# Kernel optimization log

Measured on AMD Instinct MI355X. Metric: run time of the kernel, lower is better.

## Reference

```python
import jax, jax.numpy as jnp
import numpy as np

N = 100000      # nodes
E = 2500000     # edges
DIN, H, DOUT = 3, 32, 4
EPS = 1e-5

def _lin(k, i, o):
    kw, kb = jax.random.split(k)
    lim = 1.0 / np.sqrt(i)
    W = jax.random.uniform(kw, (i, o), jnp.float32, -lim, lim)
    b = jax.random.uniform(kb, (o,), jnp.float32, -lim, lim)
    return W, b

def setup_inputs():
    key = jax.random.key(0)
    ks = jax.random.split(key, 12)
    x = jax.random.normal(ks[0], (N, DIN), jnp.float32)
    edge_index = jax.random.randint(ks[1], (2, E), 0, N, dtype=jnp.int32)
    w_in1, b_in1 = _lin(ks[2], DIN, H)
    w_in2, b_in2 = _lin(ks[3], H, H)
    gamma = jnp.ones((H,), jnp.float32)
    beta = jnp.zeros((H,), jnp.float32)
    wg1, bg1 = _lin(ks[4], H, H)
    wg2, bg2 = _lin(ks[5], H, H)
    wg3, bg3 = _lin(ks[6], H, H)
    wo1, bo1 = _lin(ks[7], H, H)
    wo2, bo2 = _lin(ks[8], H, H)
    wo3, bo3 = _lin(ks[9], H, DOUT)
    return dict(x=x, w_in1=w_in1, b_in1=b_in1, w_in2=w_in2, b_in2=b_in2,
                gamma=gamma, beta=beta,
                wg1=wg1, bg1=bg1, wg2=wg2, bg2=bg2, wg3=wg3, bg3=bg3,
                wo1=wo1, bo1=bo1, wo2=wo2, bo2=bo2, wo3=wo3, bo3=bo3,
                edge_index=edge_index)

def _gcn(h, W, b, src, dst, norm):
    # PyG GCNConv: x' = scatter_add(norm * (xW)[src] -> dst) + bias
    hw = h @ W                                   # [N, H]
    msg = hw[src] * norm[:, None]                # [E+N, H] gather + scale
    out = jax.ops.segment_sum(msg, dst, num_segments=N)
    return out + b

def reference(x, w_in1, b_in1, w_in2, b_in2, gamma, beta,
              wg1, bg1, wg2, bg2, wg3, bg3,
              wo1, bo1, wo2, bo2, wo3, bo3, edge_index):
    leaky = lambda v: jax.nn.leaky_relu(v, 0.01)
    # input MLP
    h = leaky(x @ w_in1 + b_in1)
    h = leaky(h @ w_in2 + b_in2)
    # BatchNorm1d (training-mode batch statistics, biased variance)
    mu = jnp.mean(h, axis=0)
    var = jnp.mean((h - mu) ** 2, axis=0)
    h = (h - mu) * jax.lax.rsqrt(var + EPS) * gamma + beta
    # gcn_norm with self-loops: deg over target index, sym normalization
    loop = jnp.arange(N, dtype=edge_index.dtype)
    src = jnp.concatenate([edge_index[0], loop])
    dst = jnp.concatenate([edge_index[1], loop])
    deg = jax.ops.segment_sum(jnp.ones_like(src, jnp.float32), dst, num_segments=N)
    dis = jax.lax.rsqrt(deg)                     # deg >= 1 due to self-loops
    norm = dis[src] * dis[dst]                   # [E+N]
    h = jax.nn.elu(_gcn(h, wg1, bg1, src, dst, norm))
    h = jax.nn.elu(_gcn(h, wg2, bg2, src, dst, norm))
    h = jax.nn.elu(_gcn(h, wg3, bg3, src, dst, norm))
    # output MLP
    r = leaky(h @ wo1 + bo1)
    r = leaky(r @ wo2 + bo2)
    r = r @ wo3 + bo3                            # [N, 4]
    r = r.at[:, 0].set(jax.nn.sigmoid(r[:, 0]))
    return r
```

## Files before the change

kernel.cpp:

```cpp
#include <hip/hip_runtime.h>
#include <hip/hip_fp16.h>

#define HF 32
#define EPS 1e-5f
#define BSH 8
#define BSZ 256
#define CH  4096
#define SUBCAP 1024
#define CAP (8*SUBCAP)

__device__ __forceinline__ float leaky(float v){ return fmaxf(v, 0.01f*v); }
__device__ __forceinline__ float elu1(float v){ return v > 0.f ? v : (expf(v)-1.f); }
__device__ __forceinline__ float sigmoidf(float v){ return 1.f/(1.f+expf(-v)); }

__device__ __forceinline__ void addrow8(float* a, float4 v){
    const __half2* p = (const __half2*)&v;
#pragma unroll
    for (int k = 0; k < 4; k++){
        float2 f = __half22float2(p[k]);
        a[2*k] += f.x; a[2*k+1] += f.y;
    }
}
__device__ __forceinline__ float4 h2add4f(float4 a, float4 b){
    __half2* pa = (__half2*)&a; __half2* pb = (__half2*)&b;
    float4 r; __half2* pr = (__half2*)&r;
#pragma unroll
    for (int k = 0; k < 4; k++) pr[k] = __hadd2(pa[k], pb[k]);
    return r;
}

__global__ __launch_bounds__(256)
void k_mlp(const float* __restrict__ x,
           const float* __restrict__ w1, const float* __restrict__ b1,
           const float* __restrict__ w2, const float* __restrict__ b2,
           __half* __restrict__ h, float* __restrict__ stats, int N){
    __shared__ float sW1[3*HF], sB1[HF], sW2[HF*HF], sB2[HF];
    __shared__ float sh[256][33];
    int t = threadIdx.x;
    for (int i = t; i < 3*HF; i += 256) sW1[i] = w1[i];
    if (t < HF){ sB1[t] = b1[t]; sB2[t] = b2[t]; }
    for (int i = t; i < HF*HF; i += 256) sW2[i] = w2[i];
    __syncthreads();
    int n = blockIdx.x*256 + t;
    float h2[HF];
    if (n < N){
        float x0 = x[(size_t)n*3], x1 = x[(size_t)n*3+1], x2 = x[(size_t)n*3+2];
        float h1[HF];
#pragma unroll
        for (int j = 0; j < HF; j++){
            float v = fmaf(x0, sW1[j], fmaf(x1, sW1[HF+j], fmaf(x2, sW1[2*HF+j], sB1[j])));
            h1[j] = leaky(v);
        }
#pragma unroll
        for (int j = 0; j < HF; j++){
            float v = sB2[j];
#pragma unroll
            for (int i = 0; i < HF; i++) v = fmaf(h1[i], sW2[i*HF+j], v);
            h2[j] = leaky(v);
        }
        float4* hv = (float4*)(h + (size_t)n*HF);
#pragma unroll
        for (int jb = 0; jb < 4; jb++){
            __half2 hh[4];
#pragma unroll
            for (int k = 0; k < 4; k++)
                hh[k] = __float22half2_rn(make_float2(h2[jb*8+2*k], h2[jb*8+2*k+1]));
            hv[jb] = *(float4*)hh;
        }
    } else {
#pragma unroll
        for (int j = 0; j < HF; j++) h2[j] = 0.f;
    }
#pragma unroll
    for (int j = 0; j < HF; j++) sh[t][j] = h2[j];
    __syncthreads();
    int f = t & 31, g = t >> 5;
    float s = 0.f, ss = 0.f;
    for (int i = 0; i < 32; i++){
        float v = sh[g*32 + i][f];
        s += v; ss += v*v;
    }
    __syncthreads();
    sh[g][f] = s; sh[8+g][f] = ss;
    __syncthreads();
    if (t < HF){
        float a = 0.f, b = 0.f;
#pragma unroll
        for (int g2 = 0; g2 < 8; g2++){ a += sh[g2][t]; b += sh[8+g2][t]; }
        atomicAdd(&stats[t], a);
        atomicAdd(&stats[HF+t], b);
    }
}

__global__ __launch_bounds__(256)
void k_bin(const int* __restrict__ src, const int* __restrict__ dst,
           int* __restrict__ gfill, int* __restrict__ ep, int E, int B){
    __shared__ int lcnt[512], lbase[512], lpos[512];
    int t = threadIdx.x;
    for (int i = t; i < B; i += 256){ lcnt[i] = 0; lpos[i] = 0; }
    __syncthreads();
    int base = blockIdx.x * CH;
    int xcd = blockIdx.x & 7;
#pragma unroll
    for (int i = 0; i < CH/1024; i++){
        int e = base + t + i*1024;
        int d0 = (e       < E) ? dst[e]       : -1;
        int d1 = (e+256   < E) ? dst[e+256]   : -1;
        int d2 = (e+512   < E) ? dst[e+512]   : -1;
        int d3 = (e+768   < E) ? dst[e+768]   : -1;
        if (d0 >= 0) atomicAdd(&lcnt[d0 >> BSH], 1);
        if (d1 >= 0) atomicAdd(&lcnt[d1 >> BSH], 1);
        if (d2 >= 0) atomicAdd(&lcnt[d2 >> BSH], 1);
        if (d3 >= 0) atomicAdd(&lcnt[d3 >> BSH], 1);
    }
    __syncthreads();
    for (int i = t; i < B; i += 256){
        int c = lcnt[i];
        lbase[i] = c ? (i*CAP + xcd*SUBCAP + atomicAdd(&gfill[i*8 + xcd], c)) : 0;
    }
    __syncthreads();
#pragma unroll
    for (int i = 0; i < CH/1024; i++){
        int e = base + t + i*1024;
#pragma unroll
        for (int k = 0; k < 4; k++){
            int ee = e + k*256;
            if (ee < E){
                int d = dst[ee], s = src[ee];
                int b = d >> BSH;
                int p = lbase[b] + atomicAdd(&lpos[b], 1);
                ep[p] = (s << BSH) | (d & (BSZ-1));
            }
        }
    }
}

__global__ __launch_bounds__(256)
void k_bucketD(int* __restrict__ ep, const int* __restrict__ gfill,
               int2* __restrict__ rowp2, float* __restrict__ dis, int N, int B){
    __shared__ int sep[CAP];
    __shared__ int lcnt[256], lpre[256], lfill[256], sc[256];
    int b = blockIdx.x, t = threadIdx.x;
    int cx[8], coff[8], cnt = 0;
#pragma unroll
    for (int x = 0; x < 8; x++){ cx[x] = gfill[b*8 + x]; coff[x] = cnt; cnt += cx[x]; }
    lcnt[t] = 0; lfill[t] = 0;
    __syncthreads();
    int base = b*CAP;
#pragma unroll
    for (int x = 0; x < 8; x++)
        for (int j = t; j < cx[x]; j += 256) sep[coff[x] + j] = ep[base + x*SUBCAP + j];
    __syncthreads();
    for (int e = t; e < cnt; e += 256) atomicAdd(&lcnt[sep[e] & (BSZ-1)], 1);
    __syncthreads();
    int v = lcnt[t];
    sc[t] = v; __syncthreads();
    for (int off = 1; off < 256; off <<= 1){
        int u = (t >= off) ? sc[t - off] : 0;
        __syncthreads();
        sc[t] += u;
        __syncthreads();
    }
    int pre = sc[t] - v;
    lpre[t] = pre;
    int n = b*BSZ + t;
    if (n < N){
        rowp2[n] = make_int2(base + pre, base + pre + v);
        dis[n]   = rsqrtf((float)(v + 1));
    }
    __syncthreads();
    for (int e = t; e < cnt; e += 256){
        int val = sep[e];
        int d = val & (BSZ-1);
        int p = lpre[d] + atomicAdd(&lfill[d], 1);
        ep[base + p] = val >> BSH;
    }
}

__global__ __launch_bounds__(256)
void k_bn_t1(const __half* __restrict__ h, const float* __restrict__ stats,
             const float* __restrict__ gamma, const float* __restrict__ beta,
             const float* __restrict__ W, const float* __restrict__ dis,
             __half* __restrict__ tout, int N){
    __shared__ float sW[HF*HF];
    __shared__ float sh[64][33];
    int tid = threadIdx.x;
    for (int i = tid; i < HF*HF; i += 256) sW[i] = W[i];
    int nib = tid >> 2, l = tid & 3;
    int n = blockIdx.x*64 + nib;
    float hv[8];
    float d = 0.f;
    if (n < N){
        float4 raw = ((const float4*)h)[(size_t)n*4 + l];
        const __half2* p = (const __half2*)&raw;
        float tmp[8];
#pragma unroll
        for (int k = 0; k < 4; k++){
            float2 f2 = __half22float2(p[k]);
            tmp[2*k] = f2.x; tmp[2*k+1] = f2.y;
        }
        d = dis[n];
        float inv = 1.0f / (float)N;
#pragma unroll
        for (int c = 0; c < 8; c++){
            int f = 8*l + c;
            float mu  = stats[f]    * inv;
            float var = stats[HF+f] * inv - mu*mu;
            float rs  = rsqrtf(var + EPS);
            hv[c] = (tmp[c] - mu) * rs * gamma[f] + beta[f];
        }
    } else {
#pragma unroll
        for (int c = 0; c < 8; c++) hv[c] = 0.f;
    }
    __syncthreads();
#pragma unroll
    for (int c = 0; c < 8; c++) sh[nib][8*l + c] = hv[c];
    __syncthreads();
    float o[8] = {0.f,0.f,0.f,0.f,0.f,0.f,0.f,0.f};
#pragma unroll
    for (int i = 0; i < HF; i++){
        float hvv = sh[nib][i];
        float4 w0 = *(const float4*)&sW[i*HF + 8*l];
        float4 w1 = *(const float4*)&sW[i*HF + 8*l + 4];
        o[0] = fmaf(hvv, w0.x, o[0]); o[1] = fmaf(hvv, w0.y, o[1]);
        o[2] = fmaf(hvv, w0.z, o[2]); o[3] = fmaf(hvv, w0.w, o[3]);
        o[4] = fmaf(hvv, w1.x, o[4]); o[5] = fmaf(hvv, w1.y, o[5]);
        o[6] = fmaf(hvv, w1.z, o[6]); o[7] = fmaf(hvv, w1.w, o[7]);
    }
    if (n < N){
        __half2 hh[4];
#pragma unroll
        for (int k = 0; k < 4; k++)
            hh[k] = __float22half2_rn(make_float2(o[2*k]*d, o[2*k+1]*d));
        ((float4*)tout)[(size_t)n*4 + l] = *(float4*)hh;
    }
}

__global__ __launch_bounds__(256)
void k_gather_t(const __half* __restrict__ tin, const int* __restrict__ esrc,
                const int2* __restrict__ rowp2, const float* __restrict__ dis,
                const float* __restrict__ bias, const float* __restrict__ W,
                __half* __restrict__ tout, int N){
    __shared__ float sW[HF*HF];
    __shared__ float sh[64][33];
    int tid = threadIdx.x;
    for (int i = tid; i < HF*HF; i += 256) sW[i] = W[i];
    int nib = tid >> 2, l = tid & 3;
    int n = blockIdx.x*64 + nib;
    float acc[8] = {0.f,0.f,0.f,0.f,0.f,0.f,0.f,0.f};
    float d = 0.f;
    const float4* tv = (const float4*)tin;
    if (n < N){
        addrow8(acc, tv[(size_t)n*4 + l]);
        int2 r = rowp2[n];
        int e = r.x, e1 = r.y;
        while (e < e1 && (e & 3)){ addrow8(acc, tv[(size_t)esrc[e]*4 + l]); e++; }
        for (; e + 3 < e1; e += 4){
            int4 s4 = *(const int4*)&esrc[e];
            float4 v0 = tv[(size_t)s4.x*4 + l];
            float4 v1 = tv[(size_t)s4.y*4 + l];
            float4 v2 = tv[(size_t)s4.z*4 + l];
            float4 v3 = tv[(size_t)s4.w*4 + l];
            addrow8(acc, h2add4f(h2add4f(v0, v1), h2add4f(v2, v3)));
        }
        for (; e < e1; e++) addrow8(acc, tv[(size_t)esrc[e]*4 + l]);
        d = dis[n];
#pragma unroll
        for (int c = 0; c < 8; c++)
            acc[c] = elu1(fmaf(d, acc[c], bias[8*l + c]));
    }
    __syncthreads();
#pragma unroll
    for (int c = 0; c < 8; c++) sh[nib][8*l + c] = acc[c];
    __syncthreads();
    float o[8] = {0.f,0.f,0.f,0.f,0.f,0.f,0.f,0.f};
#pragma unroll
    for (int i = 0; i < HF; i++){
        float hvv = sh[nib][i];
        float4 w0 = *(const float4*)&sW[i*HF + 8*l];
        float4 w1 = *(const float4*)&sW[i*HF + 8*l + 4];
        o[0] = fmaf(hvv, w0.x, o[0]); o[1] = fmaf(hvv, w0.y, o[1]);
        o[2] = fmaf(hvv, w0.z, o[2]); o[3] = fmaf(hvv, w0.w, o[3]);
        o[4] = fmaf(hvv, w1.x, o[4]); o[5] = fmaf(hvv, w1.y, o[5]);
        o[6] = fmaf(hvv, w1.z, o[6]); o[7] = fmaf(hvv, w1.w, o[7]);
    }
    if (n < N){
        __half2 hh[4];
#pragma unroll
        for (int k = 0; k < 4; k++)
            hh[k] = __float22half2_rn(make_float2(o[2*k]*d, o[2*k+1]*d));
        ((float4*)tout)[(size_t)n*4 + l] = *(float4*)hh;
    }
}

__global__ __launch_bounds__(256)
void k_gather_out(const __half* __restrict__ tin, const int* __restrict__ esrc,
                  const int2* __restrict__ rowp2, const float* __restrict__ dis,
                  const float* __restrict__ bg3,
                  const float* __restrict__ wo1, const float* __restrict__ bo1,
                  const float* __restrict__ wo2, const float* __restrict__ bo2,
                  const float* __restrict__ wo3, const float* __restrict__ bo3,
                  float* __restrict__ out, int N){
    __shared__ float sW1[HF*HF], sW2[HF*HF], sW3[HF*4];
    __shared__ float sh[64][33], sh2[64][33];
    int tid = threadIdx.x;
    for (int i = tid; i < HF*HF; i += 256){ sW1[i] = wo1[i]; sW2[i] = wo2[i]; }
    if (tid < HF*4) sW3[tid] = wo3[tid];
    int nib = tid >> 2, l = tid & 3;
    int n = blockIdx.x*64 + nib;
    float acc[8] = {0.f,0.f,0.f,0.f,0.f,0.f,0.f,0.f};
    const float4* tv = (const float4*)tin;
    if (n < N){
        addrow8(acc, tv[(size_t)n*4 + l]);
        int2 r = rowp2[n];
        int e = r.x, e1 = r.y;
        while (e < e1 && (e & 3)){ addrow8(acc, tv[(size_t)esrc[e]*4 + l]); e++; }
        for (; e + 3 < e1; e += 4){
            int4 s4 = *(const int4*)&esrc[e];
            float4 v0 = tv[(size_t)s4.x*4 + l];
            float4 v1 = tv[(size_t)s4.y*4 + l];
            float4 v2 = tv[(size_t)s4.z*4 + l];
            float4 v3 = tv[(size_t)s4.w*4 + l];
            addrow8(acc, h2add4f(h2add4f(v0, v1), h2add4f(v2, v3)));
        }
        for (; e < e1; e++) addrow8(acc, tv[(size_t)esrc[e]*4 + l]);
        float d = dis[n];
#pragma unroll
        for (int c = 0; c < 8; c++)
            acc[c] = elu1(fmaf(d, acc[c], bg3[8*l + c]));
    }
    __syncthreads();
#pragma unroll
    for (int c = 0; c < 8; c++) sh[nib][8*l + c] = acc[c];
    __syncthreads();
    float o1[8];
#pragma unroll
    for (int c = 0; c < 8; c++) o1[c] = bo1[8*l + c];
#pragma unroll
    for (int i = 0; i < HF; i++){
        float hvv = sh[nib][i];
        float4 w0 = *(const float4*)&sW1[i*HF + 8*l];
        float4 w1 = *(const float4*)&sW1[i*HF + 8*l + 4];
        o1[0] = fmaf(hvv, w0.x, o1[0]); o1[1] = fmaf(hvv, w0.y, o1[1]);
        o1[2] = fmaf(hvv, w0.z, o1[2]); o1[3] = fmaf(hvv, w0.w, o1[3]);
        o1[4] = fmaf(hvv, w1.x, o1[4]); o1[5] = fmaf(hvv, w1.y, o1[5]);
        o1[6] = fmaf(hvv, w1.z, o1[6]); o1[7] = fmaf(hvv, w1.w, o1[7]);
    }
#pragma unroll
    for (int c = 0; c < 8; c++) sh2[nib][8*l + c] = leaky(o1[c]);
    __syncthreads();
    float o2[8];
#pragma unroll
    for (int c = 0; c < 8; c++) o2[c] = bo2[8*l + c];
#pragma unroll
    for (int i = 0; i < HF; i++){
        float hvv = sh2[nib][i];
        float4 w0 = *(const float4*)&sW2[i*HF + 8*l];
        float4 w1 = *(const float4*)&sW2[i*HF + 8*l + 4];
        o2[0] = fmaf(hvv, w0.x, o2[0]); o2[1] = fmaf(hvv, w0.y, o2[1]);
        o2[2] = fmaf(hvv, w0.z, o2[2]); o2[3] = fmaf(hvv, w0.w, o2[3]);
        o2[4] = fmaf(hvv, w1.x, o2[4]); o2[5] = fmaf(hvv, w1.y, o2[5]);
        o2[6] = fmaf(hvv, w1.z, o2[6]); o2[7] = fmaf(hvv, w1.w, o2[7]);
    }
#pragma unroll
    for (int c = 0; c < 8; c++) sh[nib][8*l + c] = leaky(o2[c]);
    __syncthreads();
    if (n < N){
        float v = bo3[l];
#pragma unroll
        for (int i = 0; i < HF; i++) v = fmaf(sh[nib][i], sW3[i*4 + l], v);
        if (l == 0) v = sigmoidf(v);
        out[(size_t)n*4 + l] = v;
    }
}

extern "C" void kernel_launch(void* const* d_in, const int* in_sizes, int n_in,
                              void* d_out, int out_size, void* d_ws, size_t ws_size,
                              hipStream_t stream) {
    const float* x     = (const float*)d_in[0];
    const float* w_in1 = (const float*)d_in[1];
    const float* b_in1 = (const float*)d_in[2];
    const float* w_in2 = (const float*)d_in[3];
    const float* b_in2 = (const float*)d_in[4];
    const float* gamma = (const float*)d_in[5];
    const float* beta  = (const float*)d_in[6];
    const float* wg1   = (const float*)d_in[7];
    const float* bg1   = (const float*)d_in[8];
    const float* wg2   = (const float*)d_in[9];
    const float* bg2   = (const float*)d_in[10];
    const float* wg3   = (const float*)d_in[11];
    const float* bg3   = (const float*)d_in[12];
    const float* wo1   = (const float*)d_in[13];
    const float* bo1   = (const float*)d_in[14];
    const float* wo2   = (const float*)d_in[15];
    const float* bo2   = (const float*)d_in[16];
    const float* wo3   = (const float*)d_in[17];
    const float* bo3   = (const float*)d_in[18];
    const int*   ei    = (const int*)d_in[19];

    int N = in_sizes[0] / 3;
    int E = in_sizes[19] / 2;
    int B = (N + BSZ - 1) >> BSH;

    char* w = (char*)d_ws;
    size_t o = 0;
    auto alloc = [&](size_t bytes){ size_t r = o; o = (o + bytes + 255) & ~(size_t)255; return r; };
    float* stats = (float*)(w + alloc(2*HF*sizeof(float)));
    int*   gfill = (int*)  (w + alloc((size_t)B*8*4));
    size_t zero_bytes = o;
    int2*  rowp2 = (int2*) (w + alloc((size_t)N*8));
    float* dis   = (float*)(w + alloc((size_t)N*4));
    int*   ep    = (int*)  (w + alloc((size_t)B*CAP*4));
    __half* bufH = (__half*)(w + alloc((size_t)N*HF*2));
    __half* tA   = (__half*)(w + alloc((size_t)N*HF*2));
    __half* tB   = (__half*)(w + alloc((size_t)N*HF*2));

    hipMemsetAsync(d_ws, 0, zero_bytes, stream);

    const int* src = ei;
    const int* dst = ei + E;
    int NB1 = (N + 255) / 256;
    int NC  = (E + CH - 1) / CH;
    int GB  = (N + 63) / 64;

    k_mlp    <<<NB1, 256, 0, stream>>>(x, w_in1, b_in1, w_in2, b_in2, bufH, stats, N);
    k_bin    <<<NC,  256, 0, stream>>>(src, dst, gfill, ep, E, B);
    k_bucketD<<<B,   256, 0, stream>>>(ep, gfill, rowp2, dis, N, B);

    k_bn_t1   <<<GB, 256, 0, stream>>>(bufH, stats, gamma, beta, wg1, dis, tA, N);
    k_gather_t<<<GB, 256, 0, stream>>>(tA, ep, rowp2, dis, bg1, wg2, tB, N);
    k_gather_t<<<GB, 256, 0, stream>>>(tB, ep, rowp2, dis, bg2, wg3, tA, N);
    k_gather_out<<<GB, 256, 0, stream>>>(tA, ep, rowp2, dis, bg3,
                                         wo1, bo1, wo2, bo2, wo3, bo3, (float*)d_out, N);
}
```

Before: 314.6 us.

## Split feature columns into two half-planes for gather and separate dense transforms

Feature tensors are stored as two 16-column planes, and the gather kernel is split so each block aggregates one plane. Block indices are interleaved so a plane's gather traffic stays within a smaller working set that fits cache better. The 32x32 transforms and output MLP become separate kernels, which adds launches and extra round trips through memory. The binning kernel also preloads src/dst into registers once instead of reading dst twice.

```diff
diff --git a/kernel.cpp b/kernel.cpp
--- a/kernel.cpp
+++ b/kernel.cpp
@@ -101,18 +101,16 @@
     __syncthreads();
     int base = blockIdx.x * CH;
     int xcd = blockIdx.x & 7;
-#pragma unroll
-    for (int i = 0; i < CH/1024; i++){
-        int e = base + t + i*1024;
-        int d0 = (e       < E) ? dst[e]       : -1;
-        int d1 = (e+256   < E) ? dst[e+256]   : -1;
-        int d2 = (e+512   < E) ? dst[e+512]   : -1;
-        int d3 = (e+768   < E) ? dst[e+768]   : -1;
-        if (d0 >= 0) atomicAdd(&lcnt[d0 >> BSH], 1);
-        if (d1 >= 0) atomicAdd(&lcnt[d1 >> BSH], 1);
-        if (d2 >= 0) atomicAdd(&lcnt[d2 >> BSH], 1);
-        if (d3 >= 0) atomicAdd(&lcnt[d3 >> BSH], 1);
-    }
+    int dv[16], sv[16];
+#pragma unroll
+    for (int i = 0; i < 16; i++){
+        int e = base + t + i*256;
+        dv[i] = (e < E) ? dst[e] : -1;
+        sv[i] = (e < E) ? src[e] : 0;
+    }
+#pragma unroll
+    for (int i = 0; i < 16; i++)
+        if (dv[i] >= 0) atomicAdd(&lcnt[dv[i] >> BSH], 1);
     __syncthreads();
     for (int i = t; i < B; i += 256){
         int c = lcnt[i];
@@ -120,17 +118,11 @@
     }
     __syncthreads();
 #pragma unroll
-    for (int i = 0; i < CH/1024; i++){
-        int e = base + t + i*1024;
-#pragma unroll
-        for (int k = 0; k < 4; k++){
-            int ee = e + k*256;
-            if (ee < E){
-                int d = dst[ee], s = src[ee];
-                int b = d >> BSH;
-                int p = lbase[b] + atomicAdd(&lpos[b], 1);
-                ep[p] = (s << BSH) | (d & (BSZ-1));
-            }
+    for (int i = 0; i < 16; i++){
+        if (dv[i] >= 0){
+            int d = dv[i], bb = d >> BSH;
+            int p = lbase[bb] + atomicAdd(&lpos[bb], 1);
+            ep[p] = (sv[i] << BSH) | (d & (BSZ-1));
         }
     }
 }
@@ -181,7 +173,7 @@
 void k_bn_t1(const __half* __restrict__ h, const float* __restrict__ stats,
              const float* __restrict__ gamma, const float* __restrict__ beta,
              const float* __restrict__ W, const float* __restrict__ dis,
-             __half* __restrict__ tout, int N){
+             __half* __restrict__ tp0, __half* __restrict__ tp1, int N){
     __shared__ float sW[HF*HF];
     __shared__ float sh[64][33];
     int tid = threadIdx.x;
@@ -233,46 +225,79 @@
 #pragma unroll
         for (int k = 0; k < 4; k++)
             hh[k] = __float22half2_rn(make_float2(o[2*k]*d, o[2*k+1]*d));
-        ((float4*)tout)[(size_t)n*4 + l] = *(float4*)hh;
-    }
-}
-
-__global__ __launch_bounds__(256)
-void k_gather_t(const __half* __restrict__ tin, const int* __restrict__ esrc,
-                const int2* __restrict__ rowp2, const float* __restrict__ dis,
-                const float* __restrict__ bias, const float* __restrict__ W,
-                __half* __restrict__ tout, int N){
+        __half* tp = (l < 2) ? tp0 : tp1;
+        ((float4*)tp)[(size_t)n*2 + (l & 1)] = *(float4*)hh;
+    }
+}
+
+__global__ __launch_bounds__(256)
+void k_gather_s(const __half* __restrict__ tp0, const __half* __restrict__ tp1,
+                const int* __restrict__ esrc, const int2* __restrict__ rowp2,
+                const float* __restrict__ dis, const float* __restrict__ bias,
+                __half* __restrict__ hp0, __half* __restrict__ hp1, int N){
+    int b = blockIdx.x;
+    int g = (b >> 3)*4 + (b & 3);
+    int s = (b >> 2) & 1;
+    int tid = threadIdx.x;
+    int nib = tid >> 1, l = tid & 1;
+    int n = g*128 + nib;
+    if (n >= N) return;
+    const float4* tv = (const float4*)(s ? tp1 : tp0);
+    float acc[8] = {0.f,0.f,0.f,0.f,0.f,0.f,0.f,0.f};
+    addrow8(acc, tv[(size_t)n*2 + l]);
+    int2 r = rowp2[n];
+    int e = r.x, e1 = r.y;
+    while (e < e1 && (e & 3)){ addrow8(acc, tv[(size_t)esrc[e]*2 + l]); e++; }
+    for (; e + 3 < e1; e += 4){
+        int4 s4 = *(const int4*)&esrc[e];
+        float4 v0 = tv[(size_t)s4.x*2 + l];
+        float4 v1 = tv[(size_t)s4.y*2 + l];
+        float4 v2 = tv[(size_t)s4.z*2 + l];
+        float4 v3 = tv[(size_t)s4.w*2 + l];
+        addrow8(acc, h2add4f(h2add4f(v0, v1), h2add4f(v2, v3)));
+    }
+    for (; e < e1; e++) addrow8(acc, tv[(size_t)esrc[e]*2 + l]);
+    float d = dis[n];
+    const float* bs = bias + 16*s + 8*l;
+    __half2 hh[4];
+#pragma unroll
+    for (int k = 0; k < 4; k++){
+        float a = elu1(fmaf(d, acc[2*k],   bs[2*k]));
+        float bvl = elu1(fmaf(d, acc[2*k+1], bs[2*k+1]));
+        hh[k] = __float22half2_rn(make_float2(a, bvl));
+    }
+    __half* hp = s ? hp1 : hp0;
+    ((float4*)hp)[(size_t)n*2 + l] = *(float4*)hh;
+}
+
+__global__ __launch_bounds__(256)
+void k_trans(const __half* __restrict__ hp0, const __half* __restrict__ hp1,
+             const float* __restrict__ W, const float* __restrict__ dis,
+             __half* __restrict__ tp0, __half* __restrict__ tp1, int N){
     __shared__ float sW[HF*HF];
     __shared__ float sh[64][33];
     int tid = threadIdx.x;
     for (int i = tid; i < HF*HF; i += 256) sW[i] = W[i];
     int nib = tid >> 2, l = tid & 3;
     int n = blockIdx.x*64 + nib;
-    float acc[8] = {0.f,0.f,0.f,0.f,0.f,0.f,0.f,0.f};
+    float hv[8];
     float d = 0.f;
-    const float4* tv = (const float4*)tin;
-    if (n < N){
-        addrow8(acc, tv[(size_t)n*4 + l]);
-        int2 r = rowp2[n];
-        int e = r.x, e1 = r.y;
-        while (e < e1 && (e & 3)){ addrow8(acc, tv[(size_t)esrc[e]*4 + l]); e++; }
-        for (; e + 3 < e1; e += 4){
-            int4 s4 = *(const int4*)&esrc[e];
-            float4 v0 = tv[(size_t)s4.x*4 + l];
-            float4 v1 = tv[(size_t)s4.y*4 + l];
-            float4 v2 = tv[(size_t)s4.z*4 + l];
-            float4 v3 = tv[(size_t)s4.w*4 + l];
-            addrow8(acc, h2add4f(h2add4f(v0, v1), h2add4f(v2, v3)));
-        }
-        for (; e < e1; e++) addrow8(acc, tv[(size_t)esrc[e]*4 + l]);
+    if (n < N){
+        float4 raw = ((const float4*)((l < 2) ? hp0 : hp1))[(size_t)n*2 + (l & 1)];
+        const __half2* p = (const __half2*)&raw;
+#pragma unroll
+        for (int k = 0; k < 4; k++){
+            float2 f2 = __half22float2(p[k]);
+            hv[2*k] = f2.x; hv[2*k+1] = f2.y;
+        }
         d = dis[n];
-#pragma unroll
-        for (int c = 0; c < 8; c++)
-            acc[c] = elu1(fmaf(d, acc[c], bias[8*l + c]));
-    }
-    __syncthreads();
-#pragma unroll
-    for (int c = 0; c < 8; c++) sh[nib][8*l + c] = acc[c];
+    } else {
+#pragma unroll
+        for (int c = 0; c < 8; c++) hv[c] = 0.f;
+    }
+    __syncthreads();
+#pragma unroll
+    for (int c = 0; c < 8; c++) sh[nib][8*l + c] = hv[c];
     __syncthreads();
     float o[8] = {0.f,0.f,0.f,0.f,0.f,0.f,0.f,0.f};
 #pragma unroll
@@ -290,18 +315,17 @@
 #pragma unroll
         for (int k = 0; k < 4; k++)
             hh[k] = __float22half2_rn(make_float2(o[2*k]*d, o[2*k+1]*d));
-        ((float4*)tout)[(size_t)n*4 + l] = *(float4*)hh;
-    }
-}
-
-__global__ __launch_bounds__(256)
-void k_gather_out(const __half* __restrict__ tin, const int* __restrict__ esrc,
-                  const int2* __restrict__ rowp2, const float* __restrict__ dis,
-                  const float* __restrict__ bg3,
-                  const float* __restrict__ wo1, const float* __restrict__ bo1,
-                  const float* __restrict__ wo2, const float* __restrict__ bo2,
-                  const float* __restrict__ wo3, const float* __restrict__ bo3,
-                  float* __restrict__ out, int N){
+        __half* tp = (l < 2) ? tp0 : tp1;
+        ((float4*)tp)[(size_t)n*2 + (l & 1)] = *(float4*)hh;
+    }
+}
+
+__global__ __launch_bounds__(256)
+void k_out(const __half* __restrict__ hp0, const __half* __restrict__ hp1,
+           const float* __restrict__ wo1, const float* __restrict__ bo1,
+           const float* __restrict__ wo2, const float* __restrict__ bo2,
+           const float* __restrict__ wo3, const float* __restrict__ bo3,
+           float* __restrict__ out, int N){
     __shared__ float sW1[HF*HF], sW2[HF*HF], sW3[HF*4];
     __shared__ float sh[64][33], sh2[64][33];
     int tid = threadIdx.x;
@@ -309,30 +333,22 @@
     if (tid < HF*4) sW3[tid] = wo3[tid];
     int nib = tid >> 2, l = tid & 3;
     int n = blockIdx.x*64 + nib;
-    float acc[8] = {0.f,0.f,0.f,0.f,0.f,0.f,0.f,0.f};
-    const float4* tv = (const float4*)tin;
-    if (n < N){
-        addrow8(acc, tv[(size_t)n*4 + l]);
-        int2 r = rowp2[n];
-        int e = r.x, e1 = r.y;
-        while (e < e1 && (e & 3)){ addrow8(acc, tv[(size_t)esrc[e]*4 + l]); e++; }
-        for (; e + 3 < e1; e += 4){
-            int4 s4 = *(const int4*)&esrc[e];
-            float4 v0 = tv[(size_t)s4.x*4 + l];
-            float4 v1 = tv[(size_t)s4.y*4 + l];
-            float4 v2 = tv[(size_t)s4.z*4 + l];
-            float4 v3 = tv[(size_t)s4.w*4 + l];
-            addrow8(acc, h2add4f(h2add4f(v0, v1), h2add4f(v2, v3)));
-        }
-        for (; e < e1; e++) addrow8(acc, tv[(size_t)esrc[e]*4 + l]);
-        float d = dis[n];
-#pragma unroll
-        for (int c = 0; c < 8; c++)
-            acc[c] = elu1(fmaf(d, acc[c], bg3[8*l + c]));
-    }
-    __syncthreads();
-#pragma unroll
-    for (int c = 0; c < 8; c++) sh[nib][8*l + c] = acc[c];
+    float hv[8];
+    if (n < N){
+        float4 raw = ((const float4*)((l < 2) ? hp0 : hp1))[(size_t)n*2 + (l & 1)];
+        const __half2* p = (const __half2*)&raw;
+#pragma unroll
+        for (int k = 0; k < 4; k++){
+            float2 f2 = __half22float2(p[k]);
+            hv[2*k] = f2.x; hv[2*k+1] = f2.y;
+        }
+    } else {
+#pragma unroll
+        for (int c = 0; c < 8; c++) hv[c] = 0.f;
+    }
+    __syncthreads();
+#pragma unroll
+    for (int c = 0; c < 8; c++) sh[nib][8*l + c] = hv[c];
     __syncthreads();
     float o1[8];
 #pragma unroll
@@ -413,8 +429,10 @@
     float* dis   = (float*)(w + alloc((size_t)N*4));
     int*   ep    = (int*)  (w + alloc((size_t)B*CAP*4));
     __half* bufH = (__half*)(w + alloc((size_t)N*HF*2));
-    __half* tA   = (__half*)(w + alloc((size_t)N*HF*2));
-    __half* tB   = (__half*)(w + alloc((size_t)N*HF*2));
+    __half* tP0  = (__half*)(w + alloc((size_t)N*16*2));
+    __half* tP1  = (__half*)(w + alloc((size_t)N*16*2));
+    __half* hP0  = (__half*)(w + alloc((size_t)N*16*2));
+    __half* hP1  = (__half*)(w + alloc((size_t)N*16*2));
 
     hipMemsetAsync(d_ws, 0, zero_bytes, stream);
 
@@ -423,14 +441,19 @@
     int NB1 = (N + 255) / 256;
     int NC  = (E + CH - 1) / CH;
     int GB  = (N + 63) / 64;
+    int NG4 = ((N + 127) / 128 + 3) & ~3;
+    int SB  = NG4 * 2;
 
     k_mlp    <<<NB1, 256, 0, stream>>>(x, w_in1, b_in1, w_in2, b_in2, bufH, stats, N);
     k_bin    <<<NC,  256, 0, stream>>>(src, dst, gfill, ep, E, B);
     k_bucketD<<<B,   256, 0, stream>>>(ep, gfill, rowp2, dis, N, B);
 
-    k_bn_t1   <<<GB, 256, 0, stream>>>(bufH, stats, gamma, beta, wg1, dis, tA, N);
-    k_gather_t<<<GB, 256, 0, stream>>>(tA, ep, rowp2, dis, bg1, wg2, tB, N);
-    k_gather_t<<<GB, 256, 0, stream>>>(tB, ep, rowp2, dis, bg2, wg3, tA, N);
-    k_gather_out<<<GB, 256, 0, stream>>>(tA, ep, rowp2, dis, bg3,
-                                         wo1, bo1, wo2, bo2, wo3, bo3, (float*)d_out, N);
-}
+    k_bn_t1   <<<GB, 256, 0, stream>>>(bufH, stats, gamma, beta, wg1, dis, tP0, tP1, N);
+    k_gather_s<<<SB, 256, 0, stream>>>(tP0, tP1, ep, rowp2, dis, bg1, hP0, hP1, N);
+    k_trans   <<<GB, 256, 0, stream>>>(hP0, hP1, wg2, dis, tP0, tP1, N);
+    k_gather_s<<<SB, 256, 0, stream>>>(tP0, tP1, ep, rowp2, dis, bg2, hP0, hP1, N);
+    k_trans   <<<GB, 256, 0, stream>>>(hP0, hP1, wg3, dis, tP0, tP1, N);
+    k_gather_s<<<SB, 256, 0, stream>>>(tP0, tP1, ep, rowp2, dis, bg3, hP0, hP1, N);
+    k_out     <<<GB, 256, 0, stream>>>(hP0, hP1, wo1, bo1, wo2, bo2, wo3, bo3,
+                                       (float*)d_out, N);
+}
```

Result: slower. 359.2 us (+14.2%).
